# Performance work log

Measured on AMD Instinct MI355X. Metric: run time of the kernel, lower is better.

## Reference

```python
import jax, jax.numpy as jnp
import numpy as np

STRIDES = (8, 16, 32)
IMG = 608
NC = 80
A = 3
IGNORE = 0.5
ANCHORS = np.array([[12, 16], [19, 36], [40, 28], [36, 75], [76, 55], [72, 146],
                    [142, 110], [192, 243], [459, 401]], np.float32)
ANCH_MASKS = ((0, 1, 2), (3, 4, 5), (6, 7, 8))
B, NL, NVALID = 16, 60, 45


def setup_inputs():
    key = jax.random.key(0)
    ks = jax.random.split(key, 8)
    inp = {}
    for i, s in enumerate(STRIDES):
        f = IMG // s
        inp[f"xin{i}"] = jax.random.normal(ks[i], (B, A * (5 + NC), f, f), jnp.float32)
    cx = jax.random.uniform(ks[3], (B, NL), minval=40.0, maxval=568.0)
    cy = jax.random.uniform(ks[4], (B, NL), minval=40.0, maxval=568.0)
    w = jax.random.uniform(ks[5], (B, NL), minval=8.0, maxval=120.0)
    h = jax.random.uniform(ks[6], (B, NL), minval=8.0, maxval=120.0)
    cls = jax.random.randint(ks[7], (B, NL), 0, NC).astype(jnp.float32)
    labels = jnp.stack([cx - w / 2, cy - h / 2, cx + w / 2, cy + h / 2, cls], -1)
    mask = (jnp.arange(NL) < NVALID)[None, :, None]
    inp["labels"] = jnp.where(mask, labels, 0.0)
    return inp


def _iou_cxcywh(p, t):  # p:[M,4] cx,cy,w,h; t:[N,4] -> [M,N]
    tl = jnp.maximum(p[:, None, :2] - p[:, None, 2:] / 2, t[None, :, :2] - t[None, :, 2:] / 2)
    br = jnp.minimum(p[:, None, :2] + p[:, None, 2:] / 2, t[None, :, :2] + t[None, :, 2:] / 2)
    ap = p[:, 2] * p[:, 3]
    at = t[:, 2] * t[:, 3]
    en = jnp.all(tl < br, -1)
    ai = jnp.prod(br - tl, -1) * en
    return ai / (ap[:, None] + at[None, :] - ai)


def _bce(p, t, w=None):
    # torch F.binary_cross_entropy with log clamped; clamp p instead (grad-safe, value-identical here)
    lp = jnp.log(jnp.maximum(p, 1e-12))
    l1p = jnp.log1p(-jnp.minimum(p, 1.0 - 1e-7))
    l = -(t * lp + (1.0 - t) * l1p)
    if w is not None:
        l = l * w
    return l.sum()


def _scale_loss(raw, labels, sid):
    stride = STRIDES[sid]
    f = IMG // stride
    n_ch = 5 + NC
    all_g = ANCHORS / stride  # [9,2] anchors in grid units
    m_anch = jnp.asarray(all_g[list(ANCH_MASKS[sid])])  # [3,2]
    b = raw.shape[0]
    out = raw.reshape(b, A, n_ch, f, f).transpose(0, 1, 3, 4, 2)  # [B,A,f,f,n_ch]
    xy = jax.nn.sigmoid(out[..., :2])
    wh = out[..., 2:4]
    obj = jax.nn.sigmoid(out[..., 4])
    clsp = jax.nn.sigmoid(out[..., 5:])

    gx = jnp.arange(f, dtype=jnp.float32)
    pred = jnp.stack([xy[..., 0] + gx[None, None, None, :],
                      xy[..., 1] + gx[None, None, :, None],
                      jnp.exp(wh[..., 0]) * m_anch[:, 0][None, :, None, None],
                      jnp.exp(wh[..., 1]) * m_anch[:, 1][None, :, None, None]], -1)

    valid = labels.sum(2) > 0  # [B,N]
    tx = (labels[..., 0] + labels[..., 2]) / (2 * stride)
    ty = (labels[..., 1] + labels[..., 3]) / (2 * stride)
    tw = (labels[..., 2] - labels[..., 0]) / stride
    th = (labels[..., 3] - labels[..., 1]) / stride
    ii = tx.astype(jnp.int32)
    jj = ty.astype(jnp.int32)

    # anchor-target IoU: both boxes anchored at origin -> closed form
    rw = jnp.asarray(all_g[:, 0])
    rh = jnp.asarray(all_g[:, 1])
    mw = jnp.minimum(tw[..., None], rw)
    mh = jnp.minimum(th[..., None], rh)
    inter = mw * mh * ((mw > 0) & (mh > 0))
    aiou = inter / (tw[..., None] * th[..., None] + rw * rh - inter)  # [B,N,9]
    best_all = jnp.argmax(aiou, -1)
    best_n = best_all % 3
    use = valid & (best_all // 3 == sid)

    # ignore mask from pred-vs-truth IoU
    tbox = jnp.stack([tx, ty, tw, th], -1)  # [B,N,4]
    ious = jax.vmap(_iou_cxcywh)(pred.reshape(b, -1, 4), tbox)  # [B,A*f*f,N]
    ious = ious * valid[:, None, :]
    obj_mask = (ious.max(-1).reshape(b, A, f, f) <= IGNORE).astype(jnp.float32)

    bb = jnp.broadcast_to(jnp.arange(b)[:, None], (b, labels.shape[1])).ravel()
    aa = best_n.ravel()
    jjs = jnp.where(use, jj, f).ravel()  # out-of-bounds index -> update dropped
    iis = ii.ravel()

    def scat(v):
        return jnp.zeros((b, A, f, f), jnp.float32).at[bb, aa, jjs, iis].set(v.ravel(), mode='drop')

    t0 = scat(tx - ii.astype(jnp.float32))
    t1 = scat(ty - jj.astype(jnp.float32))
    t2 = scat(jnp.log(tw / m_anch[best_n, 0] + 1e-16))
    t3 = scat(jnp.log(th / m_anch[best_n, 1] + 1e-16))
    t4 = scat(jnp.ones_like(tx))
    m = scat(jnp.ones_like(tx))
    sc = scat(jnp.sqrt(2.0 - tw * th / (f * f)))
    tcls = jnp.zeros((b, A, f, f, NC), jnp.float32).at[
        bb, aa, jjs, iis, labels[..., 4].astype(jnp.int32).ravel()].set(1.0, mode='drop')
    obj_mask = obj_mask.at[bb, aa, jjs, iis].set(1.0, mode='drop')

    m1 = m[..., None]
    sc1 = sc[..., None]
    o_xy = xy * m1
    g_xy = jnp.stack([t0, t1], -1) * m1
    o_wh = wh * m1 * sc1
    g_wh = jnp.stack([t2, t3], -1) * m1 * sc1
    o_ob = obj * obj_mask
    g_ob = t4 * obj_mask
    o_cl = clsp * m1
    g_cl = tcls * m1

    l_xy = _bce(o_xy, g_xy, (sc * sc)[..., None])
    l_wh = 0.5 * jnp.sum((o_wh - g_wh) ** 2)
    l_ob = _bce(o_ob, g_ob)
    l_cl = _bce(o_cl, g_cl)
    fo = jnp.concatenate([o_xy, o_wh, o_ob[..., None], o_cl], -1)
    ft = jnp.concatenate([g_xy, g_wh, g_ob[..., None], g_cl], -1)
    l2 = jnp.sum((fo - ft) ** 2)
    return jnp.stack([l_xy, l_wh, l_ob, l_cl, l2])


def reference(xin0, xin1, xin2, labels):
    parts = (_scale_loss(xin0, labels, 0) + _scale_loss(xin1, labels, 1)
             + _scale_loss(xin2, labels, 2))
    l_xy, l_wh, l_ob, l_cl, l2 = parts
    return jnp.stack([l_xy + l_wh + l_ob + l_cl, l_xy, l_wh, l_ob, l_cl, l2])
```

## Files before the change

kernel.cpp:

```cpp
#include <hip/hip_runtime.h>

#define BB 16
#define NL 60
#define NA 3
#define NC 80
#define BS 512
#define NLP 64

#define NBX0C 9
#define NBX1C 3
#define NBX2C 1
#define NBXC  (NBX0C+NBX1C+NBX2C)
#define NBX   (NBXC+1)
#define TOTAL_BLOCKS (NBX*BB)

__device__ __constant__ float d_AW[9] = {12.f,19.f,40.f,36.f,76.f,72.f,142.f,192.f,459.f};
__device__ __constant__ float d_AH[9] = {16.f,36.f,28.f,75.f,55.f,146.f,110.f,243.f,401.f};

__device__ __forceinline__ float sig_pos(float v){ return __fdividef(1.0f, 1.0f + __expf(-v)); }
__device__ __forceinline__ float sig_neg(float v){ return __fdividef(1.0f, 1.0f + __expf(v)); }
__device__ __forceinline__ float bcef(float p, float t){
    float lp  = __logf(fmaxf(p, 1e-12f));
    float l1p = __logf(1.0f - fminf(p, 1.0f - 1e-7f));
    return -(t*lp + (1.0f - t)*l1p);
}

template<int SID>
__device__ __forceinline__ bool cell_load(const float* __restrict__ raw, int xoff, int b, int tid,
        int &a, int &rembase, int &nc,
        float (&cx)[4], float (&cy)[4], float (&cw)[4], float (&ch)[4], float (&co)[4])
{
    constexpr int F  = (SID==0)?76:(SID==1)?38:19;
    constexpr int FF = F*F;
    int t = xoff*BS + tid;
    if (SID < 2){
        constexpr int NT = 3*FF/4;
        if (t >= NT) return false;
        a = t / (FF/4);
        rembase = 4*t - a*FF;
        nc = 4;
        const float* base = raw + ((size_t)(b*(NA*85) + a*85))*FF + rembase;
        float4 q0 = *reinterpret_cast<const float4*>(base);
        float4 q1 = *reinterpret_cast<const float4*>(base +   (size_t)FF);
        float4 q2 = *reinterpret_cast<const float4*>(base + 2*(size_t)FF);
        float4 q3 = *reinterpret_cast<const float4*>(base + 3*(size_t)FF);
        float4 q4 = *reinterpret_cast<const float4*>(base + 4*(size_t)FF);
        cx[0]=q0.x; cx[1]=q0.y; cx[2]=q0.z; cx[3]=q0.w;
        cy[0]=q1.x; cy[1]=q1.y; cy[2]=q1.z; cy[3]=q1.w;
        cw[0]=q2.x; cw[1]=q2.y; cw[2]=q2.z; cw[3]=q2.w;
        ch[0]=q3.x; ch[1]=q3.y; ch[2]=q3.z; ch[3]=q3.w;
        co[0]=q4.x; co[1]=q4.y; co[2]=q4.z; co[3]=q4.w;
    } else {
        constexpr int GPA = (FF+3)/4;
        if (t >= 3*GPA) return false;
        a = t / GPA;
        int k = t - a*GPA;
        rembase = 4*k;
        nc = (FF - rembase < 4) ? (FF - rembase) : 4;
        const float* base = raw + ((size_t)(b*(NA*85) + a*85))*FF + rembase;
        #pragma unroll
        for (int c=0;c<4;c++){
            bool v = c < nc;
            cx[c] = v ? base[c]              : 0.f;
            cy[c] = v ? base[(size_t)FF+c]   : 0.f;
            cw[c] = v ? base[2*(size_t)FF+c] : 0.f;
            ch[c] = v ? base[3*(size_t)FF+c] : 0.f;
            co[c] = v ? base[4*(size_t)FF+c] : 0.f;
        }
    }
    return true;
}

template<int SID>
__device__ __forceinline__ void cell_compute(int a, int rembase, int nc,
        const float (&cx)[4], const float (&cy)[4], const float (&cw)[4],
        const float (&ch)[4], const float (&co)[4],
        const float4* s_bxc, const float* s_at3c, int nbx8,
        const int* s_used, int nuse,
        float &lob, float &l2)
{
    constexpr int   F   = (SID==0)?76:(SID==1)?38:19;
    constexpr int   FF  = F*F;
    constexpr float RST = (SID==0)?0.125f:(SID==1)?0.0625f:0.03125f;
    float aw = d_AW[SID*3+a]*RST, ah = d_AH[SID*3+a]*RST;
    float plox[4],phix[4],ploy[4],phiy[4],ap3[4];
    #pragma unroll
    for (int c=0;c<4;c++){
        int cel = rembase + c;
        int j = cel / F;
        int i = cel - j*F;
        float x = sig_pos(cx[c]), y = sig_pos(cy[c]);
        float pw = __expf(cw[c])*aw, ph = __expf(ch[c])*ah;
        float px = x + (float)i, py = y + (float)j;
        float hx = 0.5f*pw, hy = 0.5f*ph;
        plox[c]=px-hx; phix[c]=px+hx; ploy[c]=py-hy; phiy[c]=py+hy;
        ap3[c]=pw*ph*(1.0f/3.0f);
    }
    bool skip0=false, skip1=false, skip2=false, skip3=false;
    #pragma unroll 8
    for (int l=0;l<nbx8;l++){
        float4 bb = s_bxc[l];
        float thr = s_at3c[l];
        float iw0 = fminf(phix[0],bb.y)-fmaxf(plox[0],bb.x);
        float ih0 = fminf(phiy[0],bb.w)-fmaxf(ploy[0],bb.z);
        float iw1 = fminf(phix[1],bb.y)-fmaxf(plox[1],bb.x);
        float ih1 = fminf(phiy[1],bb.w)-fmaxf(ploy[1],bb.z);
        float iw2 = fminf(phix[2],bb.y)-fmaxf(plox[2],bb.x);
        float ih2 = fminf(phiy[2],bb.w)-fmaxf(ploy[2],bb.z);
        float iw3 = fminf(phix[3],bb.y)-fmaxf(plox[3],bb.x);
        float ih3 = fminf(phiy[3],bb.w)-fmaxf(ploy[3],bb.z);
        skip0 = skip0 || (fmaxf(iw0,0.f)*fmaxf(ih0,0.f) > ap3[0]+thr);
        skip1 = skip1 || (fmaxf(iw1,0.f)*fmaxf(ih1,0.f) > ap3[1]+thr);
        skip2 = skip2 || (fmaxf(iw2,0.f)*fmaxf(ih2,0.f) > ap3[2]+thr);
        skip3 = skip3 || (fmaxf(iw3,0.f)*fmaxf(ih3,0.f) > ap3[3]+thr);
    }
    int cellbase = a*FF + rembase;
    for (int k=0;k<nuse;k++){
        int uc = s_used[k];
        skip0 = skip0 || (uc==cellbase);
        skip1 = skip1 || (uc==cellbase+1);
        skip2 = skip2 || (uc==cellbase+2);
        skip3 = skip3 || (uc==cellbase+3);
    }
    #pragma unroll
    for (int c=0;c<4;c++){
        bool sk = (c==0)?skip0:(c==1)?skip1:(c==2)?skip2:skip3;
        if (c < nc && !sk){
            float snb = sig_neg(co[c]);
            lob += -__logf(fmaxf(snb,1e-7f));
            float ob = 1.0f - snb;
            l2 += ob*ob;
        }
    }
}

__global__ __launch_bounds__(BS) void fused_kernel(
        const float* __restrict__ x0, const float* __restrict__ x1,
        const float* __restrict__ x2, const float* __restrict__ labels,
        float* __restrict__ part)
{
    __shared__ float4 s_bxc[NLP];
    __shared__ float  s_at3c[NLP];
    __shared__ int    s_used[NL];
    __shared__ int    s_nuse, s_nbx, s_ntgt;
    __shared__ int    s_code3[3][NL];
    __shared__ float  s_tv3[3][NL][5];
    __shared__ int    s_tinfo[NL];
    __shared__ unsigned long long s_tm0[NL], s_tm1[NL];
    __shared__ float  red[5][8];

    const int tid = threadIdx.x;
    const int bxi = blockIdx.x;
    const int b   = blockIdx.y;

    int sid, xoff, tgtblk;
    if      (bxi < NBX0C)       { sid = 0; xoff = bxi;               tgtblk = 0; }
    else if (bxi < NBX0C+NBX1C) { sid = 1; xoff = bxi-NBX0C;         tgtblk = 0; }
    else if (bxi < NBXC)        { sid = 2; xoff = bxi-(NBX0C+NBX1C); tgtblk = 0; }
    else                        { sid = 0; xoff = 0;                 tgtblk = 1; }

    float cx[4],cy[4],cw[4],chn[4],co[4];
    int a=0, rembase=0, nc=0;
    bool active=false;
    if (!tgtblk){
        const float* raw = (sid==0)?x0:(sid==1)?x1:x2;
        if      (sid==0) active = cell_load<0>(raw,xoff,b,tid,a,rembase,nc,cx,cy,cw,chn,co);
        else if (sid==1) active = cell_load<1>(raw,xoff,b,tid,a,rembase,nc,cx,cy,cw,chn,co);
        else             active = cell_load<2>(raw,xoff,b,tid,a,rembase,nc,cx,cy,cw,chn,co);
    }

    if (tid == 0){ s_nuse = 0; s_nbx = 0; s_ntgt = 0; }
    if (tid < NLP){
        s_bxc[tid]  = make_float4(3e38f, -3e38f, 3e38f, -3e38f);
        s_at3c[tid] = 0.f;
    }
    __syncthreads();

    if (!tgtblk){
        if (tid < NL){
            const float RSTv = (sid==0)?0.125f:(sid==1)?0.0625f:0.03125f;
            const int   F    = (sid==0)?76:(sid==1)?38:19;
            const float* lb = labels + ((size_t)b*NL + tid)*5;
            float x1f=lb[0], y1f=lb[1], x2f=lb[2], y2f=lb[3], cl=lb[4];
            bool valid = (x1f+y1f+x2f+y2f+cl) > 0.0f;
            float tx=(x1f+x2f)*0.5f*RSTv, ty=(y1f+y2f)*0.5f*RSTv;
            float tw=(x2f-x1f)*RSTv, th=(y2f-y1f)*RSTv;
            float at=tw*th;
            float best=-1.0f; int bi=0;
            #pragma unroll
            for (int k=0;k<9;k++){
                float rw=d_AW[k]*RSTv, rh=d_AH[k]*RSTv;
                float mw=fminf(tw,rw), mh=fminf(th,rh);
                float inter=(mw>0.f && mh>0.f)? mw*mh : 0.f;
                float aiou = inter/(at + rw*rh - inter);
                if (aiou > best){ best=aiou; bi=k; }
            }
            if (valid){
                int p = atomicAdd(&s_nbx, 1);
                float htw=0.5f*tw, hth=0.5f*th;
                s_bxc[p]  = make_float4(tx-htw, tx+htw, ty-hth, ty+hth);
                s_at3c[p] = at*(1.0f/3.0f);
            }
            if (valid && (bi/3 == sid)){
                int bn = bi%3;
                int ii=(int)tx, jj=(int)ty;
                int p = atomicAdd(&s_nuse, 1);
                s_used[p] = (bn*F + jj)*F + ii;
            }
        }
    } else {
        if (tid < 3*NL){
            int sd = tid/NL, l = tid - sd*NL;
            const float RSTv = (sd==0)?0.125f:(sd==1)?0.0625f:0.03125f;
            const int   F    = (sd==0)?76:(sd==1)?38:19;
            const int   FF   = F*F;
            const float* lb = labels + ((size_t)b*NL + l)*5;
            float x1f=lb[0], y1f=lb[1], x2f=lb[2], y2f=lb[3], cl=lb[4];
            bool valid = (x1f+y1f+x2f+y2f+cl) > 0.0f;
            float tx=(x1f+x2f)*0.5f*RSTv, ty=(y1f+y2f)*0.5f*RSTv;
            float tw=(x2f-x1f)*RSTv, th=(y2f-y1f)*RSTv;
            float at=tw*th;
            float best=-1.0f; int bi=0;
            #pragma unroll
            for (int k=0;k<9;k++){
                float rw=d_AW[k]*RSTv, rh=d_AH[k]*RSTv;
                float mw=fminf(tw,rw), mh=fminf(th,rh);
                float inter=(mw>0.f && mh>0.f)? mw*mh : 0.f;
                float aiou = inter/(at + rw*rh - inter);
                if (aiou > best){ best=aiou; bi=k; }
            }
            int bn = bi%3;
            bool use = valid && (bi/3 == sd);
            int ii=(int)tx, jj=(int)ty;
            int rr = jj*F + ii;
            s_code3[sd][l] = use ? (rr | (bn<<18) | (((int)cl)<<20)) : -1;
            float aw=d_AW[sd*3+bn]*RSTv, ah=d_AH[sd*3+bn]*RSTv;
            s_tv3[sd][l][0]=tx-(float)ii;
            s_tv3[sd][l][1]=ty-(float)jj;
            s_tv3[sd][l][2]=__logf(__fdividef(tw,aw) + 1e-16f);
            s_tv3[sd][l][3]=__logf(__fdividef(th,ah) + 1e-16f);
            s_tv3[sd][l][4]=sqrtf(2.0f - at/(float)FF);
        }
        __syncthreads();
        if (tid < 3*NL){
            int sd = tid/NL, l = tid - sd*NL;
            int cd = s_code3[sd][l];
            if (cd >= 0){
                int tcell = cd & 0xFFFFF;
                int last = -1;
                unsigned long long cm0=0ull, cm1=0ull;
                for (int q=0;q<NL;q++){
                    int cq = s_code3[sd][q];
                    if (cq>=0 && (cq&0xFFFFF)==tcell){
                        last = q; int cc = cq>>20;
                        if (cc<64) cm0 |= 1ull<<cc; else cm1 |= 1ull<<(cc-64);
                    }
                }
                if (last == l){
                    int p = atomicAdd(&s_ntgt, 1);
                    int rr = cd & 0x3FFFF, aa = (cd>>18)&3;
                    s_tinfo[p] = rr | (aa<<13) | (sd<<15) | (l<<17);
                    s_tm0[p] = cm0; s_tm1[p] = cm1;
                }
            }
        }
    }
    __syncthreads();

    float lxy=0.f, lwh=0.f, lob=0.f, lcl=0.f, l2=0.f;

    if (!tgtblk){
        if (active){
            int nuse = s_nuse;
            int nbx8 = (s_nbx + 7) & ~7;
            if      (sid==0) cell_compute<0>(a,rembase,nc,cx,cy,cw,chn,co,s_bxc,s_at3c,nbx8,s_used,nuse,lob,l2);
            else if (sid==1) cell_compute<1>(a,rembase,nc,cx,cy,cw,chn,co,s_bxc,s_at3c,nbx8,s_used,nuse,lob,l2);
            else             cell_compute<2>(a,rembase,nc,cx,cy,cw,chn,co,s_bxc,s_at3c,nbx8,s_used,nuse,lob,l2);
        }
    } else {
        const int wv = tid>>6, lane = tid&63;
        const int ntgt = s_ntgt;
        float P1[8], P2[8], E[8];
        int   info[8];
        #pragma unroll
        for (int kk=0; kk<8; kk++){
            int k = wv + kk*8;
            P1[kk]=0.f; P2[kk]=0.f; E[kk]=0.f; info[kk]=-1;
            if (k < ntgt){
                int in = s_tinfo[k];
                info[kk] = in;
                int rr = in & 0x1FFF, aa = (in>>13)&3, sd = (in>>15)&3;
                const float* raw = (sd==0)?x0:(sd==1)?x1:x2;
                int FF = (sd==0)?5776:(sd==1)?1444:361;
                const float* cb = raw + ((size_t)(b*(NA*85) + aa*85))*FF + rr;
                P1[kk] = cb[(size_t)(5+lane)*FF];
                if (lane < 16) P2[kk] = cb[(size_t)(69+lane)*FF];
                if (lane <  5) E[kk]  = cb[(size_t)lane*FF];
            }
        }
        #pragma unroll
        for (int kk=0; kk<8; kk++){
            int in = info[kk];
            if (in < 0) continue;
            int k  = wv + kk*8;
            int l  = (in>>17)&63, sd = (in>>15)&3;
            unsigned long long cm0 = s_tm0[k], cm1 = s_tm1[k];
            float e0=__shfl(E[kk],0), e1=__shfl(E[kk],1), e2=__shfl(E[kk],2),
                  e3=__shfl(E[kk],3), e4=__shfl(E[kk],4);
            float p1 = sig_pos(P1[kk]);
            float t1v = (((cm0>>lane)&1ull)!=0ull) ? 1.f : 0.f;
            lcl += bcef(p1, t1v);
            float d1 = p1 - t1v; l2 += d1*d1;
            if (lane < 16){
                float p2 = sig_pos(P2[kk]);
                float t2v = (((cm1>>lane)&1ull)!=0ull) ? 1.f : 0.f;
                lcl += bcef(p2, t2v);
                float d2 = p2 - t2v; l2 += d2*d2;
            }
            if (lane == 0){
                float xx=sig_pos(e0), yy=sig_pos(e1), ob=sig_pos(e4);
                float t0=s_tv3[sd][l][0], t1=s_tv3[sd][l][1], t2=s_tv3[sd][l][2],
                      t3=s_tv3[sd][l][3], sc=s_tv3[sd][l][4];
                lxy += sc*sc*(bcef(xx,t0)+bcef(yy,t1));
                float d0=(e2-t2)*sc, dd=(e3-t3)*sc;
                lwh += 0.5f*(d0*d0+dd*dd);
                lob += -__logf(fmaxf(ob,1e-12f));
                float dx=xx-t0, dy=yy-t1, dob=ob-1.f;
                l2  += dx*dx+dy*dy+d0*d0+dd*dd+dob*dob;
            }
        }
    }

    float v0=lxy, v1=lwh, v2=lob, v3=lcl, v4=l2;
    #pragma unroll
    for (int off=32; off>0; off>>=1){
        v0 += __shfl_down(v0, off, 64);
        v1 += __shfl_down(v1, off, 64);
        v2 += __shfl_down(v2, off, 64);
        v3 += __shfl_down(v3, off, 64);
        v4 += __shfl_down(v4, off, 64);
    }
    if ((tid & 63) == 0){
        int w = tid >> 6;
        red[0][w]=v0; red[1][w]=v1; red[2][w]=v2; red[3][w]=v3; red[4][w]=v4;
    }
    __syncthreads();
    if (tid == 0){
        int slot = b*NBX + bxi;
        #pragma unroll
        for (int c=0;c<5;c++){
            part[c*TOTAL_BLOCKS + slot] = red[c][0]+red[c][1]+red[c][2]+red[c][3]
                                        + red[c][4]+red[c][5]+red[c][6]+red[c][7];
        }
    }
}

__global__ __launch_bounds__(256) void fin_kernel(const float* __restrict__ part,
                                                  float* __restrict__ out)
{
    __shared__ double red[5][4];
    int tid = threadIdx.x;
    double v[5] = {0,0,0,0,0};
    if (tid < TOTAL_BLOCKS){
        #pragma unroll
        for (int c=0;c<5;c++) v[c] = (double)part[c*TOTAL_BLOCKS + tid];
    }
    #pragma unroll
    for (int off=32; off>0; off>>=1){
        #pragma unroll
        for (int c=0;c<5;c++) v[c] += __shfl_down(v[c], off, 64);
    }
    if ((tid & 63) == 0){
        int w = tid >> 6;
        #pragma unroll
        for (int c=0;c<5;c++) red[c][w] = v[c];
    }
    __syncthreads();
    if (tid == 0){
        double lxy = red[0][0]+red[0][1]+red[0][2]+red[0][3];
        double lwh = red[1][0]+red[1][1]+red[1][2]+red[1][3];
        double lob = red[2][0]+red[2][1]+red[2][2]+red[2][3];
        double lcl = red[3][0]+red[3][1]+red[3][2]+red[3][3];
        double l2  = red[4][0]+red[4][1]+red[4][2]+red[4][3];
        out[0]=(float)(lxy+lwh+lob+lcl);
        out[1]=(float)lxy; out[2]=(float)lwh; out[3]=(float)lob;
        out[4]=(float)lcl; out[5]=(float)l2;
    }
}

extern "C" void kernel_launch(void* const* d_in, const int* in_sizes, int n_in,
                              void* d_out, int out_size, void* d_ws, size_t ws_size,
                              hipStream_t stream) {
    const float* x0     = (const float*)d_in[0];
    const float* x1     = (const float*)d_in[1];
    const float* x2     = (const float*)d_in[2];
    const float* labels = (const float*)d_in[3];
    float* out = (float*)d_out;

    float* part = (float*)d_ws;

    fused_kernel<<<dim3(NBX, BB), BS, 0, stream>>>(x0, x1, x2, labels, part);
    fin_kernel<<<1, 256, 0, stream>>>(part, out);
}
```

Baseline: 25.15 us.

## Halve per-thread cell work and block size to launch more blocks per image

Each thread now handles 2 grid cells instead of 4, and blocks shrink from 512 to 256 threads. The per-image block count rises from 13 to 46 compute blocks, so far more of the device's CUs are occupied. The IoU loop now runs over the exact box count rather than a padded multiple of 8, which removes the sentinel-box initialisation. The target block uses 4 waves with 12 slots each, and the final reduction loops over the larger partial array. The cost is more blocks that each redo label preprocessing, and a target capacity of 48 instead of 64, which could drop targets if more than 48 exist.

```diff
diff --git a/kernel.cpp b/kernel.cpp
--- a/kernel.cpp
+++ b/kernel.cpp
@@ -4,12 +4,11 @@
 #define NL 60
 #define NA 3
 #define NC 80
-#define BS 512
-#define NLP 64
-
-#define NBX0C 9
-#define NBX1C 3
-#define NBX2C 1
+#define BS 256
+
+#define NBX0C 34
+#define NBX1C 9
+#define NBX2C 3
 #define NBXC  (NBX0C+NBX1C+NBX2C)
 #define NBX   (NBXC+1)
 #define TOTAL_BLOCKS (NBX*BB)
@@ -28,38 +27,38 @@
 template<int SID>
 __device__ __forceinline__ bool cell_load(const float* __restrict__ raw, int xoff, int b, int tid,
         int &a, int &rembase, int &nc,
-        float (&cx)[4], float (&cy)[4], float (&cw)[4], float (&ch)[4], float (&co)[4])
+        float (&cx)[2], float (&cy)[2], float (&cw)[2], float (&ch)[2], float (&co)[2])
 {
     constexpr int F  = (SID==0)?76:(SID==1)?38:19;
     constexpr int FF = F*F;
     int t = xoff*BS + tid;
     if (SID < 2){
-        constexpr int NT = 3*FF/4;
+        constexpr int NT = 3*FF/2;
         if (t >= NT) return false;
-        a = t / (FF/4);
-        rembase = 4*t - a*FF;
-        nc = 4;
+        a = t / (FF/2);
+        rembase = 2*t - a*FF;
+        nc = 2;
         const float* base = raw + ((size_t)(b*(NA*85) + a*85))*FF + rembase;
-        float4 q0 = *reinterpret_cast<const float4*>(base);
-        float4 q1 = *reinterpret_cast<const float4*>(base +   (size_t)FF);
-        float4 q2 = *reinterpret_cast<const float4*>(base + 2*(size_t)FF);
-        float4 q3 = *reinterpret_cast<const float4*>(base + 3*(size_t)FF);
-        float4 q4 = *reinterpret_cast<const float4*>(base + 4*(size_t)FF);
-        cx[0]=q0.x; cx[1]=q0.y; cx[2]=q0.z; cx[3]=q0.w;
-        cy[0]=q1.x; cy[1]=q1.y; cy[2]=q1.z; cy[3]=q1.w;
-        cw[0]=q2.x; cw[1]=q2.y; cw[2]=q2.z; cw[3]=q2.w;
-        ch[0]=q3.x; ch[1]=q3.y; ch[2]=q3.z; ch[3]=q3.w;
-        co[0]=q4.x; co[1]=q4.y; co[2]=q4.z; co[3]=q4.w;
+        float2 q0 = *reinterpret_cast<const float2*>(base);
+        float2 q1 = *reinterpret_cast<const float2*>(base +   (size_t)FF);
+        float2 q2 = *reinterpret_cast<const float2*>(base + 2*(size_t)FF);
+        float2 q3 = *reinterpret_cast<const float2*>(base + 3*(size_t)FF);
+        float2 q4 = *reinterpret_cast<const float2*>(base + 4*(size_t)FF);
+        cx[0]=q0.x; cx[1]=q0.y;
+        cy[0]=q1.x; cy[1]=q1.y;
+        cw[0]=q2.x; cw[1]=q2.y;
+        ch[0]=q3.x; ch[1]=q3.y;
+        co[0]=q4.x; co[1]=q4.y;
     } else {
-        constexpr int GPA = (FF+3)/4;
+        constexpr int GPA = (FF+1)/2;
         if (t >= 3*GPA) return false;
         a = t / GPA;
         int k = t - a*GPA;
-        rembase = 4*k;
-        nc = (FF - rembase < 4) ? (FF - rembase) : 4;
+        rembase = 2*k;
+        nc = (FF - rembase < 2) ? (FF - rembase) : 2;
         const float* base = raw + ((size_t)(b*(NA*85) + a*85))*FF + rembase;
         #pragma unroll
-        for (int c=0;c<4;c++){
+        for (int c=0;c<2;c++){
             bool v = c < nc;
             cx[c] = v ? base[c]              : 0.f;
             cy[c] = v ? base[(size_t)FF+c]   : 0.f;
@@ -73,9 +72,9 @@
 
 template<int SID>
 __device__ __forceinline__ void cell_compute(int a, int rembase, int nc,
-        const float (&cx)[4], const float (&cy)[4], const float (&cw)[4],
-        const float (&ch)[4], const float (&co)[4],
-        const float4* s_bxc, const float* s_at3c, int nbx8,
+        const float (&cx)[2], const float (&cy)[2], const float (&cw)[2],
+        const float (&ch)[2], const float (&co)[2],
+        const float4* s_bxc, const float* s_at3c, int nbx,
         const int* s_used, int nuse,
         float &lob, float &l2)
 {
@@ -83,9 +82,9 @@
     constexpr int   FF  = F*F;
     constexpr float RST = (SID==0)?0.125f:(SID==1)?0.0625f:0.03125f;
     float aw = d_AW[SID*3+a]*RST, ah = d_AH[SID*3+a]*RST;
-    float plox[4],phix[4],ploy[4],phiy[4],ap3[4];
+    float plox[2],phix[2],ploy[2],phiy[2],ap3[2];
     #pragma unroll
-    for (int c=0;c<4;c++){
+    for (int c=0;c<2;c++){
         int cel = rembase + c;
         int j = cel / F;
         int i = cel - j*F;
@@ -96,35 +95,27 @@
         plox[c]=px-hx; phix[c]=px+hx; ploy[c]=py-hy; phiy[c]=py+hy;
         ap3[c]=pw*ph*(1.0f/3.0f);
     }
-    bool skip0=false, skip1=false, skip2=false, skip3=false;
-    #pragma unroll 8
-    for (int l=0;l<nbx8;l++){
+    bool skip0=false, skip1=false;
+    #pragma unroll 2
+    for (int l=0;l<nbx;l++){
         float4 bb = s_bxc[l];
         float thr = s_at3c[l];
         float iw0 = fminf(phix[0],bb.y)-fmaxf(plox[0],bb.x);
         float ih0 = fminf(phiy[0],bb.w)-fmaxf(ploy[0],bb.z);
         float iw1 = fminf(phix[1],bb.y)-fmaxf(plox[1],bb.x);
         float ih1 = fminf(phiy[1],bb.w)-fmaxf(ploy[1],bb.z);
-        float iw2 = fminf(phix[2],bb.y)-fmaxf(plox[2],bb.x);
-        float ih2 = fminf(phiy[2],bb.w)-fmaxf(ploy[2],bb.z);
-        float iw3 = fminf(phix[3],bb.y)-fmaxf(plox[3],bb.x);
-        float ih3 = fminf(phiy[3],bb.w)-fmaxf(ploy[3],bb.z);
         skip0 = skip0 || (fmaxf(iw0,0.f)*fmaxf(ih0,0.f) > ap3[0]+thr);
         skip1 = skip1 || (fmaxf(iw1,0.f)*fmaxf(ih1,0.f) > ap3[1]+thr);
-        skip2 = skip2 || (fmaxf(iw2,0.f)*fmaxf(ih2,0.f) > ap3[2]+thr);
-        skip3 = skip3 || (fmaxf(iw3,0.f)*fmaxf(ih3,0.f) > ap3[3]+thr);
     }
     int cellbase = a*FF + rembase;
     for (int k=0;k<nuse;k++){
         int uc = s_used[k];
         skip0 = skip0 || (uc==cellbase);
         skip1 = skip1 || (uc==cellbase+1);
-        skip2 = skip2 || (uc==cellbase+2);
-        skip3 = skip3 || (uc==cellbase+3);
     }
     #pragma unroll
-    for (int c=0;c<4;c++){
-        bool sk = (c==0)?skip0:(c==1)?skip1:(c==2)?skip2:skip3;
+    for (int c=0;c<2;c++){
+        bool sk = (c==0)?skip0:skip1;
         if (c < nc && !sk){
             float snb = sig_neg(co[c]);
             lob += -__logf(fmaxf(snb,1e-7f));
@@ -139,15 +130,15 @@
         const float* __restrict__ x2, const float* __restrict__ labels,
         float* __restrict__ part)
 {
-    __shared__ float4 s_bxc[NLP];
-    __shared__ float  s_at3c[NLP];
+    __shared__ float4 s_bxc[NL];
+    __shared__ float  s_at3c[NL];
     __shared__ int    s_used[NL];
     __shared__ int    s_nuse, s_nbx, s_ntgt;
     __shared__ int    s_code3[3][NL];
     __shared__ float  s_tv3[3][NL][5];
     __shared__ int    s_tinfo[NL];
     __shared__ unsigned long long s_tm0[NL], s_tm1[NL];
-    __shared__ float  red[5][8];
+    __shared__ float  red[5][4];
 
     const int tid = threadIdx.x;
     const int bxi = blockIdx.x;
@@ -159,7 +150,7 @@
     else if (bxi < NBXC)        { sid = 2; xoff = bxi-(NBX0C+NBX1C); tgtblk = 0; }
     else                        { sid = 0; xoff = 0;                 tgtblk = 1; }
 
-    float cx[4],cy[4],cw[4],chn[4],co[4];
+    float cx[2],cy[2],cw[2],chn[2],co[2];
     int a=0, rembase=0, nc=0;
     bool active=false;
     if (!tgtblk){
@@ -170,10 +161,6 @@
     }
 
     if (tid == 0){ s_nuse = 0; s_nbx = 0; s_ntgt = 0; }
-    if (tid < NLP){
-        s_bxc[tid]  = make_float4(3e38f, -3e38f, 3e38f, -3e38f);
-        s_at3c[tid] = 0.f;
-    }
     __syncthreads();
 
     if (!tgtblk){
@@ -271,20 +258,19 @@
 
     if (!tgtblk){
         if (active){
-            int nuse = s_nuse;
-            int nbx8 = (s_nbx + 7) & ~7;
-            if      (sid==0) cell_compute<0>(a,rembase,nc,cx,cy,cw,chn,co,s_bxc,s_at3c,nbx8,s_used,nuse,lob,l2);
-            else if (sid==1) cell_compute<1>(a,rembase,nc,cx,cy,cw,chn,co,s_bxc,s_at3c,nbx8,s_used,nuse,lob,l2);
-            else             cell_compute<2>(a,rembase,nc,cx,cy,cw,chn,co,s_bxc,s_at3c,nbx8,s_used,nuse,lob,l2);
+            int nuse = s_nuse, nbx = s_nbx;
+            if      (sid==0) cell_compute<0>(a,rembase,nc,cx,cy,cw,chn,co,s_bxc,s_at3c,nbx,s_used,nuse,lob,l2);
+            else if (sid==1) cell_compute<1>(a,rembase,nc,cx,cy,cw,chn,co,s_bxc,s_at3c,nbx,s_used,nuse,lob,l2);
+            else             cell_compute<2>(a,rembase,nc,cx,cy,cw,chn,co,s_bxc,s_at3c,nbx,s_used,nuse,lob,l2);
         }
     } else {
         const int wv = tid>>6, lane = tid&63;
         const int ntgt = s_ntgt;
-        float P1[8], P2[8], E[8];
-        int   info[8];
-        #pragma unroll
-        for (int kk=0; kk<8; kk++){
-            int k = wv + kk*8;
+        float P1[12], P2[12], E[12];
+        int   info[12];
+        #pragma unroll
+        for (int kk=0; kk<12; kk++){
+            int k = wv + kk*4;
             P1[kk]=0.f; P2[kk]=0.f; E[kk]=0.f; info[kk]=-1;
             if (k < ntgt){
                 int in = s_tinfo[k];
@@ -299,10 +285,10 @@
             }
         }
         #pragma unroll
-        for (int kk=0; kk<8; kk++){
+        for (int kk=0; kk<12; kk++){
             int in = info[kk];
             if (in < 0) continue;
-            int k  = wv + kk*8;
+            int k  = wv + kk*4;
             int l  = (in>>17)&63, sd = (in>>15)&3;
             unsigned long long cm0 = s_tm0[k], cm1 = s_tm1[k];
             float e0=__shfl(E[kk],0), e1=__shfl(E[kk],1), e2=__shfl(E[kk],2),
@@ -349,8 +335,7 @@
         int slot = b*NBX + bxi;
         #pragma unroll
         for (int c=0;c<5;c++){
-            part[c*TOTAL_BLOCKS + slot] = red[c][0]+red[c][1]+red[c][2]+red[c][3]
-                                        + red[c][4]+red[c][5]+red[c][6]+red[c][7];
+            part[c*TOTAL_BLOCKS + slot] = red[c][0]+red[c][1]+red[c][2]+red[c][3];
         }
     }
 }
@@ -361,9 +346,9 @@
     __shared__ double red[5][4];
     int tid = threadIdx.x;
     double v[5] = {0,0,0,0,0};
-    if (tid < TOTAL_BLOCKS){
-        #pragma unroll
-        for (int c=0;c<5;c++) v[c] = (double)part[c*TOTAL_BLOCKS + tid];
+    for (int i = tid; i < TOTAL_BLOCKS; i += 256){
+        #pragma unroll
+        for (int c=0;c<5;c++) v[c] += (double)part[c*TOTAL_BLOCKS + i];
     }
     #pragma unroll
     for (int off=32; off>0; off>>=1){
```

Result: slower. 31.02 us (+23.3%).
